# Optimization experiments

Hardware: AMD Instinct MI355X
Metric: run time of the kernel (lower is better)

## Reference

```python
import jax, jax.numpy as jnp
from jax import lax
import numpy as np

N, T, V, C, K, NIN, TSTEPS = 4096, 1, 26, 256, 3, 9, 25


def setup_inputs() -> dict:
    key = jax.random.key(0)
    ks = jax.random.split(key, 28)
    s = 0.02
    inp = {
        "inputs": jax.random.normal(ks[0], (N, T, V * 3), jnp.float32),
        "inputs_previous": jax.random.normal(ks[1], (N, T, V * 3), jnp.float32),
        "inputs_previous2": jax.random.normal(ks[2], (N, T, V * 3), jnp.float32),
        "hidden": jax.random.normal(ks[3], (N, C, V), jnp.float32),
        # graph adjacency buffer [k_num, V, V] (non-trainable) + edge weights
        "A": jax.random.uniform(ks[4], (K, V, V), jnp.float32),
        "emul": jnp.ones((K, V, V), jnp.float32),
        "eadd": jnp.ones((K, V, V), jnp.float32),
        # DecodeGcn conv1d kernel_size=1 -> stored as [C*K, C] matrix
        "conv_w": jax.random.normal(ks[5], (C * K, C), jnp.float32) * s,
        "conv_b": jnp.zeros((C * K,), jnp.float32),
        # GRU input projections (bias=True), Linear(n_in_dec=9 -> C)
        "Wir": jax.random.normal(ks[6], (C, NIN), jnp.float32) * s,
        "bir": jnp.zeros((C,), jnp.float32),
        "Wii": jax.random.normal(ks[7], (C, NIN), jnp.float32) * s,
        "bii": jnp.zeros((C,), jnp.float32),
        "Win": jax.random.normal(ks[8], (C, NIN), jnp.float32) * s,
        "b_in": jnp.zeros((C,), jnp.float32),
        # GRU hidden projections (bias=False)
        "Whr": jax.random.normal(ks[9], (C, C), jnp.float32) * s,
        "Whi": jax.random.normal(ks[10], (C, C), jnp.float32) * s,
        "Whh": jax.random.normal(ks[11], (C, C), jnp.float32) * s,
        # output MLP head
        "W1": jax.random.normal(ks[12], (C, C), jnp.float32) * s,
        "b1": jnp.zeros((C,), jnp.float32),
        "W2": jax.random.normal(ks[13], (C, C), jnp.float32) * s,
        "b2": jnp.zeros((C,), jnp.float32),
        "W3": jax.random.normal(ks[14], (3, C), jnp.float32) * s,
        "b3": jnp.zeros((3,), jnp.float32),
        "t": TSTEPS,
    }
    return inp


def reference(inputs, inputs_previous, inputs_previous2, hidden, A, emul, eadd,
              conv_w, conv_b, Wir, bir, Wii, bii, Win, b_in, Whr, Whi, Whh,
              W1, b1, W2, b2, W3, b3, t):
    n_batch, n_t, d = inputs.shape
    v = A.shape[1]
    k_num = A.shape[0]
    c = hidden.shape[1]

    x0 = inputs.reshape(n_batch, n_t, v, -1)[:, 0]            # [N,V,3]
    xp = inputs_previous.reshape(n_batch, n_t, v, -1)[:, 0]   # [N,V,3]
    xp2 = inputs_previous2.reshape(n_batch, n_t, v, -1)[:, 0]  # [N,V,3]

    A_adj = A * emul + eadd  # [k,V,V]
    # noise injected on position channels each step (torch.randn * 0.0005)
    noise = jax.random.normal(jax.random.key(1), (t, n_batch, v, 3), jnp.float32) * 5e-4

    def gcn(h):  # h: [N,C,V] -> [N,C,V]   (kernel-size-1 conv + graph einsum)
        y = jnp.einsum('ncv,oc->nov', h, conv_w) + conv_b[None, :, None]  # [N,C*k,V]
        y = y.reshape(n_batch, k_num, c, v)
        return jnp.einsum('nkcv,kvw->ncw', y, A_adj)

    def step(carry, inp):
        hid, h1, h2, h3 = carry  # hid: [N,C,V]; h1/h2/h3: last three predictions [N,V,3]
        s, nz = inp
        msg = lax.cond(s < 10, gcn, lambda h: h, hid)  # [N,C,V]
        # unified history recurrence (covers step 0/1/2/>=3 branches):
        ins_p = h1
        ins_v = h2 - h3
        ins_a = ins_p - h2 - ins_v
        x = jnp.concatenate([ins_p + nz, ins_v, ins_a], axis=-1)  # [N,V,9]
        m = msg.transpose(0, 2, 1)       # [N,V,C]
        hprev = hid.transpose(0, 2, 1)   # [N,V,C]
        r = jax.nn.sigmoid(x @ Wir.T + bir + m @ Whr.T)
        z = jax.nn.sigmoid(x @ Wii.T + bii + m @ Whi.T)
        nn_ = jnp.tanh(x @ Win.T + b_in + r * (m @ Whh.T))
        hnew = (1.0 - z) * nn_ + z * hprev  # [N,V,C]
        # output MLP (dropout in eval mode = identity), leaky_relu slope 0.1
        hd = jax.nn.leaky_relu(hnew @ W1.T + b1, 0.1)
        hd = jax.nn.leaky_relu(hd @ W2.T + b2, 0.1)
        res = hd @ W3.T + b3                 # [N,V,3]
        pred = x[:, :, :3] + res             # pred_ = (ins_p + noise) + residual
        return (hnew.transpose(0, 2, 1), pred, h1, h2), pred

    init = (hidden, x0, xp, xp2)
    _, preds = lax.scan(step, init, (jnp.arange(t), noise))  # preds: [t,N,V,3]
    return preds.transpose(1, 2, 0, 3)  # [N,V,t,3] == preds.transpose(1,2) in torch
```

## Files before the change

kernel.cpp:

```cpp
#include <hip/hip_runtime.h>

#define M_ROWS 106496
#define NBATCH 4096
#define VN 26
#define KNUM 3
#define TS 25

typedef unsigned short u16;
typedef __attribute__((ext_vector_type(8))) short v8s;
typedef __attribute__((ext_vector_type(4))) float v4f;

__device__ __forceinline__ u16 f2bf(float f) {
    unsigned u = __float_as_uint(f);
    u += 0x7FFF + ((u >> 16) & 1);
    return (u16)(u >> 16);
}
__device__ __forceinline__ float bf2f(u16 h) {
    return __uint_as_float(((unsigned)h) << 16);
}
__device__ __forceinline__ float sigm(float x) {
    return 1.f / (1.f + __expf(-x));
}
__device__ __forceinline__ float tanh_fast(float x) {
    return 2.f / (1.f + __expf(-2.f * x)) - 1.f;
}

typedef const __attribute__((address_space(1))) unsigned int* gas_t;
typedef __attribute__((address_space(3))) unsigned int* las_t;
__device__ __forceinline__ void gl16(const void* g, void* l) {
    __builtin_amdgcn_global_load_lds((gas_t)g, (las_t)l, 16, 0, 0);
}

template <int ACT>
__global__ __launch_bounds__(256) void gemm_nt(
    const u16* __restrict__ A, const u16* __restrict__ Bt,
    const float* __restrict__ bias, u16* __restrict__ C, int nc)
{
    __shared__ u16 Al[2][128 * 32];
    __shared__ u16 Bl[2][128 * 32];
    const int m0 = blockIdx.x * 128;
    const int n0 = blockIdx.y * 128;
    const int tid = threadIdx.x;
    const int wid = tid >> 6, lane = tid & 63;
    const int ln = lane & 15, q = lane >> 4;
    const int qs8 = (q ^ ((ln >> 1) & 3)) * 8;
    const int wm = (wid >> 1) * 64, wn = (wid & 1) * 64;
    const int srow = tid >> 2;
    const int spart = (tid & 3) ^ ((srow >> 1) & 3);

    const u16* gA0 = &A[(size_t)(m0 + srow) * 256 + spart * 8];
    const u16* gB0 = &Bt[(size_t)(n0 + srow) * 256 + spart * 8];

#define STG(b, kk) do {                                                     \
        gl16(gA0 + (kk) * 32,            &Al[b][wid * 512]);                \
        gl16(gA0 + 64 * 256 + (kk) * 32, &Al[b][2048 + wid * 512]);         \
        gl16(gB0 + (kk) * 32,            &Bl[b][wid * 512]);                \
        gl16(gB0 + 64 * 256 + (kk) * 32, &Bl[b][2048 + wid * 512]);         \
    } while (0)

    v4f acc[4][4] = {};
    STG(0, 0);
    __syncthreads();
#pragma unroll
    for (int kt = 0; kt < 8; ++kt) {
        const int cb = kt & 1, nb = cb ^ 1;
        if (kt < 7) STG(nb, kt + 1);
        v8s af[4], bfv[4];
#pragma unroll
        for (int i = 0; i < 4; ++i)
            af[i] = *(const v8s*)&Al[cb][(wm + i * 16 + ln) * 32 + qs8];
#pragma unroll
        for (int j = 0; j < 4; ++j)
            bfv[j] = *(const v8s*)&Bl[cb][(wn + j * 16 + ln) * 32 + qs8];
#pragma unroll
        for (int i = 0; i < 4; ++i)
#pragma unroll
            for (int j = 0; j < 4; ++j)
                acc[i][j] = __builtin_amdgcn_mfma_f32_16x16x32_bf16(
                    af[i], bfv[j], acc[i][j], 0, 0, 0);
        __syncthreads();
    }
#undef STG
#pragma unroll
    for (int i = 0; i < 4; ++i)
#pragma unroll
        for (int j = 0; j < 4; ++j) {
            int gc = n0 + wn + j * 16 + ln;
            float b = bias[gc];
#pragma unroll
            for (int r = 0; r < 4; ++r) {
                int gr = m0 + wm + i * 16 + q * 4 + r;
                float v = acc[i][j][r] + b;
                if (ACT) v = v > 0.f ? v : 0.1f * v;
                C[(size_t)gr * nc + gc] = f2bf(v);
            }
        }
}

__global__ __launch_bounds__(256) void gemm_head(
    const u16* __restrict__ A, const u16* __restrict__ Bt,
    const float* __restrict__ bias, const float* __restrict__ w3,
    float* __restrict__ resp0, float* __restrict__ resp1)
{
    __shared__ u16 Al[2][128 * 32];
    __shared__ u16 Bl[2][128 * 32];
    __shared__ float w3l[3 * 128];
    __shared__ float resl[2][128][3];
    const int m0 = blockIdx.x * 128;
    const int by = blockIdx.y;
    const int n0 = by * 128;
    const int tid = threadIdx.x;
    const int wid = tid >> 6, lane = tid & 63;
    const int ln = lane & 15, q = lane >> 4;
    const int qs8 = (q ^ ((ln >> 1) & 3)) * 8;
    const int wm = (wid >> 1) * 64, wn = (wid & 1) * 64;
    const int wnh = wid & 1;
    const int srow = tid >> 2;
    const int spart = (tid & 3) ^ ((srow >> 1) & 3);

    for (int idx = tid; idx < 384; idx += 256)
        w3l[idx] = w3[(idx >> 7) * 256 + n0 + (idx & 127)];

    const u16* gA0 = &A[(size_t)(m0 + srow) * 256 + spart * 8];
    const u16* gB0 = &Bt[(size_t)(n0 + srow) * 256 + spart * 8];

#define STG(b, kk) do {                                                     \
        gl16(gA0 + (kk) * 32,            &Al[b][wid * 512]);                \
        gl16(gA0 + 64 * 256 + (kk) * 32, &Al[b][2048 + wid * 512]);         \
        gl16(gB0 + (kk) * 32,            &Bl[b][wid * 512]);                \
        gl16(gB0 + 64 * 256 + (kk) * 32, &Bl[b][2048 + wid * 512]);         \
    } while (0)

    v4f acc[4][4] = {};
    STG(0, 0);
    __syncthreads();
#pragma unroll
    for (int kt = 0; kt < 8; ++kt) {
        const int cb = kt & 1, nb = cb ^ 1;
        if (kt < 7) STG(nb, kt + 1);
        v8s af[4], bfv[4];
#pragma unroll
        for (int i = 0; i < 4; ++i)
            af[i] = *(const v8s*)&Al[cb][(wm + i * 16 + ln) * 32 + qs8];
#pragma unroll
        for (int j = 0; j < 4; ++j)
            bfv[j] = *(const v8s*)&Bl[cb][(wn + j * 16 + ln) * 32 + qs8];
#pragma unroll
        for (int i = 0; i < 4; ++i)
#pragma unroll
            for (int j = 0; j < 4; ++j)
                acc[i][j] = __builtin_amdgcn_mfma_f32_16x16x32_bf16(
                    af[i], bfv[j], acc[i][j], 0, 0, 0);
        __syncthreads();
    }
#undef STG

    float bj[4], wv[3][4];
#pragma unroll
    for (int j = 0; j < 4; ++j) {
        bj[j] = bias[n0 + wn + j * 16 + ln];
#pragma unroll
        for (int t = 0; t < 3; ++t)
            wv[t][j] = w3l[t * 128 + wn + j * 16 + ln];
    }
#pragma unroll
    for (int i = 0; i < 4; ++i) {
        float part[3][4] = {};
#pragma unroll
        for (int j = 0; j < 4; ++j)
#pragma unroll
            for (int r = 0; r < 4; ++r) {
                float v = acc[i][j][r] + bj[j];
                v = v > 0.f ? v : 0.1f * v;
                part[0][r] += v * wv[0][j];
                part[1][r] += v * wv[1][j];
                part[2][r] += v * wv[2][j];
            }
#pragma unroll
        for (int off = 1; off < 16; off <<= 1)
#pragma unroll
            for (int t = 0; t < 3; ++t)
#pragma unroll
                for (int r = 0; r < 4; ++r)
                    part[t][r] += __shfl_xor(part[t][r], off, 16);
        if (ln == 0) {
            int row = wm + i * 16 + q * 4;
#pragma unroll
            for (int r = 0; r < 4; ++r)
#pragma unroll
                for (int t = 0; t < 3; ++t)
                    resl[wnh][row + r][t] = part[t][r];
        }
    }
    __syncthreads();
    float* rp = by ? resp1 : resp0;
    for (int idx = tid; idx < 384; idx += 256) {
        int t = idx >> 7, row = idx & 127;
        rp[(size_t)(m0 + row) * 3 + t] = resl[0][row][t] + resl[1][row][t];
    }
}

__global__ __launch_bounds__(256) void head_fin(
    const float* __restrict__ resp0, const float* __restrict__ resp1,
    const float* __restrict__ b3, const float* __restrict__ p1,
    const float* __restrict__ p2, float* __restrict__ pnew,
    u16* __restrict__ xpad, float* __restrict__ out, int s)
{
    int m = blockIdx.x * 256 + threadIdx.x;
    float s0 = resp0[m * 3 + 0] + resp1[m * 3 + 0];
    float s1 = resp0[m * 3 + 1] + resp1[m * 3 + 1];
    float s2 = resp0[m * 3 + 2] + resp1[m * 3 + 2];
    float a0 = p1[m * 3 + 0], a1 = p1[m * 3 + 1], a2 = p1[m * 3 + 2];
    float c0 = p2[m * 3 + 0], c1 = p2[m * 3 + 1], c2 = p2[m * 3 + 2];
    float o0 = a0 + s0 + b3[0];
    float o1 = a1 + s1 + b3[1];
    float o2 = a2 + s2 + b3[2];
    size_t ob = ((size_t)m * TS + s) * 3;
    out[ob + 0] = o0; out[ob + 1] = o1; out[ob + 2] = o2;
    pnew[m * 3 + 0] = o0; pnew[m * 3 + 1] = o1; pnew[m * 3 + 2] = o2;
    unsigned t[32];
#pragma unroll
    for (int i = 0; i < 32; ++i) t[i] = 0;
    t[0] = f2bf(o0); t[1] = f2bf(o1); t[2] = f2bf(o2);
    t[3] = f2bf(a0 - c0); t[4] = f2bf(a1 - c1); t[5] = f2bf(a2 - c2);
    t[6] = f2bf(o0 - 2.f * a0 + c0);
    t[7] = f2bf(o1 - 2.f * a1 + c1);
    t[8] = f2bf(o2 - 2.f * a2 + c2);
    t[9] = f2bf(1.f);
    uint4* dst = (uint4*)&xpad[(size_t)m * 32];
#pragma unroll
    for (int wq = 0; wq < 4; ++wq) {
        uint4 u;
        u.x = t[wq * 8 + 0] | (t[wq * 8 + 1] << 16);
        u.y = t[wq * 8 + 2] | (t[wq * 8 + 3] << 16);
        u.z = t[wq * 8 + 4] | (t[wq * 8 + 5] << 16);
        u.w = t[wq * 8 + 6] | (t[wq * 8 + 7] << 16);
        dst[wq] = u;
    }
}

__global__ __launch_bounds__(256) void graph_mix(
    const u16* __restrict__ y, const float* __restrict__ aadj,
    u16* __restrict__ msg)
{
    __shared__ u16 yl[VN * 768];
    const int n = blockIdx.x, tid = threadIdx.x;
    const uint4* src = (const uint4*)(y + (size_t)n * VN * 768);
    for (int idx = tid; idx < VN * 768 / 8; idx += 256)
        ((uint4*)yl)[idx] = src[idx];
    __syncthreads();
    const int c = tid;
    float acc[VN] = {};
    for (int k = 0; k < KNUM; ++k)
        for (int v = 0; v < VN; ++v) {
            float yv = bf2f(yl[v * 768 + k * 256 + c]);
            const float* ap = &aadj[(k * VN + v) * VN];
#pragma unroll
            for (int w = 0; w < VN; ++w) acc[w] += yv * ap[w];
        }
    size_t base = (size_t)n * VN * 256;
    for (int w = 0; w < VN; ++w) msg[base + w * 256 + c] = f2bf(acc[w]);
}

__global__ __launch_bounds__(256) void gru_fused(
    const u16* __restrict__ Am, const u16* __restrict__ xpad,
    const u16* __restrict__ hprev, u16* __restrict__ hout,
    const u16* __restrict__ wfull, const u16* __restrict__ wxn)
{
    __shared__ u16 Al[128 * 32];
    __shared__ u16 Bl[192 * 32];
    __shared__ u16 Xl[64 * 32];
    const int m0 = blockIdx.x * 128;
    const int n0 = blockIdx.y * 64;
    const int tid = threadIdx.x;
    const int wid = tid >> 6, lane = tid & 63;
    const int ln = lane & 15, q = lane >> 4;
    const int qs8 = (q ^ ((ln >> 1) & 3)) * 8;
    const int wm = (wid >> 1) * 64, wn = (wid & 1) * 32;
    const int srow = tid >> 2;
    const int spart = (tid & 3) ^ ((srow >> 1) & 3);

    gl16(&wxn[(size_t)(n0 + srow) * 32 + spart * 8], &Xl[(wid * 64) * 8]);

    v4f accr[4][2] = {}, accz[4][2] = {}, acch[4][2] = {}, accn[4][2] = {};

    for (int kt = 0; kt < 9; ++kt) {
#pragma unroll
        for (int p = 0; p < 2; ++p) {
            const u16* ga = (kt < 8)
                ? &Am[(size_t)(m0 + p * 64 + srow) * 256 + kt * 32 + spart * 8]
                : &xpad[(size_t)(m0 + p * 64 + srow) * 32 + spart * 8];
            gl16(ga, &Al[(p * 256 + wid * 64) * 8]);
        }
#pragma unroll
        for (int p = 0; p < 3; ++p)
            gl16(&wfull[(size_t)(p * 256 + n0 + srow) * 288 + kt * 32 + spart * 8],
                 &Bl[(p * 256 + wid * 64) * 8]);
        __syncthreads();

        v8s af[4];
#pragma unroll
        for (int i = 0; i < 4; ++i)
            af[i] = *(const v8s*)&Al[(wm + i * 16 + ln) * 32 + qs8];
        v8s bfr[3][2];
#pragma unroll
        for (int g = 0; g < 3; ++g)
#pragma unroll
            for (int j = 0; j < 2; ++j)
                bfr[g][j] = *(const v8s*)&Bl[(g * 64 + wn + j * 16 + ln) * 32 + qs8];
#pragma unroll
        for (int i = 0; i < 4; ++i)
#pragma unroll
            for (int j = 0; j < 2; ++j) {
                accr[i][j] = __builtin_amdgcn_mfma_f32_16x16x32_bf16(af[i], bfr[0][j], accr[i][j], 0, 0, 0);
                accz[i][j] = __builtin_amdgcn_mfma_f32_16x16x32_bf16(af[i], bfr[1][j], accz[i][j], 0, 0, 0);
                acch[i][j] = __builtin_amdgcn_mfma_f32_16x16x32_bf16(af[i], bfr[2][j], acch[i][j], 0, 0, 0);
            }
        if (kt == 8) {
            v8s bfn[2];
#pragma unroll
            for (int j = 0; j < 2; ++j)
                bfn[j] = *(const v8s*)&Xl[(wn + j * 16 + ln) * 32 + qs8];
#pragma unroll
            for (int i = 0; i < 4; ++i)
#pragma unroll
                for (int j = 0; j < 2; ++j)
                    accn[i][j] = __builtin_amdgcn_mfma_f32_16x16x32_bf16(af[i], bfn[j], accn[i][j], 0, 0, 0);
        }
        __syncthreads();
    }

#pragma unroll
    for (int i = 0; i < 4; ++i)
#pragma unroll
        for (int j = 0; j < 2; ++j) {
            int gc = n0 + wn + j * 16 + ln;
#pragma unroll
            for (int r = 0; r < 4; ++r) {
                int gr = m0 + wm + i * 16 + q * 4 + r;
                float rg = sigm(accr[i][j][r]);
                float zg = sigm(accz[i][j][r]);
                float nn = tanh_fast(accn[i][j][r] + rg * acch[i][j][r]);
                float hp = bf2f(hprev[(size_t)gr * 256 + gc]);
                hout[(size_t)gr * 256 + gc] = f2bf((1.f - zg) * nn + zg * hp);
            }
        }
}

__global__ __launch_bounds__(256) void init_xpad(
    const float* __restrict__ x0, const float* __restrict__ xp,
    const float* __restrict__ xp2, u16* __restrict__ xpad)
{
    int m = blockIdx.x * 256 + threadIdx.x;
    float a0 = x0[m * 3 + 0], a1 = x0[m * 3 + 1], a2 = x0[m * 3 + 2];
    float b0 = xp[m * 3 + 0], b1 = xp[m * 3 + 1], b2 = xp[m * 3 + 2];
    float c0 = xp2[m * 3 + 0], c1 = xp2[m * 3 + 1], c2 = xp2[m * 3 + 2];
    unsigned t[32];
#pragma unroll
    for (int i = 0; i < 32; ++i) t[i] = 0;
    t[0] = f2bf(a0); t[1] = f2bf(a1); t[2] = f2bf(a2);
    t[3] = f2bf(b0 - c0); t[4] = f2bf(b1 - c1); t[5] = f2bf(b2 - c2);
    t[6] = f2bf(a0 - 2.f * b0 + c0);
    t[7] = f2bf(a1 - 2.f * b1 + c1);
    t[8] = f2bf(a2 - 2.f * b2 + c2);
    t[9] = f2bf(1.f);
    uint4* dst = (uint4*)&xpad[(size_t)m * 32];
#pragma unroll
    for (int wq = 0; wq < 4; ++wq) {
        uint4 u;
        u.x = t[wq * 8 + 0] | (t[wq * 8 + 1] << 16);
        u.y = t[wq * 8 + 2] | (t[wq * 8 + 3] << 16);
        u.z = t[wq * 8 + 4] | (t[wq * 8 + 5] << 16);
        u.w = t[wq * 8 + 6] | (t[wq * 8 + 7] << 16);
        dst[wq] = u;
    }
}

__global__ __launch_bounds__(256) void transpose_h(
    const float* __restrict__ hidden, u16* __restrict__ hA)
{
    __shared__ float hl[256 * VN];
    const int n = blockIdx.x, tid = threadIdx.x;
    const uint4* src = (const uint4*)(hidden + (size_t)n * 256 * VN);
    for (int idx = tid; idx < 256 * VN / 4; idx += 256)
        ((uint4*)hl)[idx] = src[idx];
    __syncthreads();
    size_t base = (size_t)n * VN * 256;
    for (int idx = tid; idx < VN * 256; idx += 256) {
        int v = idx >> 8, c = idx & 255;
        hA[base + idx] = f2bf(hl[c * VN + v]);
    }
}

__global__ __launch_bounds__(256) void pack_weights(
    const float* __restrict__ Whr, const float* __restrict__ Whi,
    const float* __restrict__ Whh, const float* __restrict__ convw_f,
    const float* __restrict__ W1f, const float* __restrict__ W2f,
    const float* __restrict__ Af, const float* __restrict__ emul,
    const float* __restrict__ eadd, const float* __restrict__ Wir,
    const float* __restrict__ Wii, const float* __restrict__ Win,
    const float* __restrict__ bir, const float* __restrict__ bii,
    const float* __restrict__ b_in, const float* __restrict__ convb_f,
    const float* __restrict__ b1f, const float* __restrict__ b2f,
    const float* __restrict__ W3f, const float* __restrict__ b3f,
    u16* __restrict__ wfull, u16* __restrict__ wxn, u16* __restrict__ convw,
    u16* __restrict__ w1, u16* __restrict__ w2, float* __restrict__ aadj,
    float* __restrict__ convb, float* __restrict__ b1, float* __restrict__ b2,
    float* __restrict__ w3, float* __restrict__ b3)
{
    int gid = blockIdx.x * 256 + threadIdx.x;
    int stride = gridDim.x * 256;
    for (int i = gid; i < 768 * 288; i += stride) {
        int row = i / 288, col = i - row * 288;
        int g = row >> 8, c = row & 255;
        float v = 0.f;
        if (col < 256)
            v = (g == 0 ? Whr : (g == 1 ? Whi : Whh))[c * 256 + col];
        else if (col < 265) {
            int tcol = col - 256;
            v = (g == 0 ? Wir[c * 9 + tcol] : (g == 1 ? Wii[c * 9 + tcol] : 0.f));
        } else if (col == 265)
            v = (g == 0 ? bir[c] : (g == 1 ? bii[c] : 0.f));
        wfull[i] = f2bf(v);
    }
    for (int i = gid; i < 256 * 32; i += stride) {
        int c = i >> 5, col = i & 31;
        float v = 0.f;
        if (col < 9) v = Win[c * 9 + col];
        else if (col == 9) v = b_in[c];
        wxn[i] = f2bf(v);
    }
    for (int i = gid; i < 65536; i += stride) {
        w1[i] = f2bf(W1f[i]);
        w2[i] = f2bf(W2f[i]);
    }
    for (int i = gid; i < 196608; i += stride) convw[i] = f2bf(convw_f[i]);
    for (int i = gid; i < KNUM * VN * VN; i += stride)
        aadj[i] = Af[i] * emul[i] + eadd[i];
    for (int i = gid; i < 256; i += stride) { b1[i] = b1f[i]; b2[i] = b2f[i]; }
    for (int i = gid; i < 768; i += stride) { convb[i] = convb_f[i]; w3[i] = W3f[i]; }
    if (gid < 3) b3[gid] = b3f[gid];
}

extern "C" void kernel_launch(void* const* d_in, const int* in_sizes, int n_in,
                              void* d_out, int out_size, void* d_ws, size_t ws_size,
                              hipStream_t stream)
{
    const float* inputs   = (const float*)d_in[0];
    const float* inputs_p = (const float*)d_in[1];
    const float* inputs_p2= (const float*)d_in[2];
    const float* hidden   = (const float*)d_in[3];
    const float* Af       = (const float*)d_in[4];
    const float* emul     = (const float*)d_in[5];
    const float* eadd     = (const float*)d_in[6];
    const float* conv_w   = (const float*)d_in[7];
    const float* conv_b   = (const float*)d_in[8];
    const float* Wir      = (const float*)d_in[9];
    const float* bir      = (const float*)d_in[10];
    const float* Wii      = (const float*)d_in[11];
    const float* bii      = (const float*)d_in[12];
    const float* Win      = (const float*)d_in[13];
    const float* b_in     = (const float*)d_in[14];
    const float* Whr      = (const float*)d_in[15];
    const float* Whi      = (const float*)d_in[16];
    const float* Whh      = (const float*)d_in[17];
    const float* W1f      = (const float*)d_in[18];
    const float* b1f      = (const float*)d_in[19];
    const float* W2f      = (const float*)d_in[20];
    const float* b2f      = (const float*)d_in[21];
    const float* W3f      = (const float*)d_in[22];
    const float* b3f      = (const float*)d_in[23];
    float* out = (float*)d_out;

    const size_t M = M_ROWS;
    char* ws = (char*)d_ws;
    size_t off = 0;
    auto alloc = [&](size_t bytes) -> void* {
        void* p = ws + off;
        off = (off + bytes + 255) & ~(size_t)255;
        return p;
    };
    u16* hA    = (u16*)alloc(M * 256 * 2);
    u16* hB    = (u16*)alloc(M * 256 * 2);
    u16* msg   = (u16*)alloc(M * 256 * 2);
    u16* ybuf  = (u16*)alloc(M * 768 * 2);
    u16* xpad  = (u16*)alloc(M * 32 * 2);
    float* pa  = (float*)alloc(M * 3 * 4);
    float* pb  = (float*)alloc(M * 3 * 4);
    float* pc  = (float*)alloc(M * 3 * 4);
    float* rs0 = (float*)alloc(M * 3 * 4);
    float* rs1 = (float*)alloc(M * 3 * 4);
    u16* wfull = (u16*)alloc(768 * 288 * 2);
    u16* wxn   = (u16*)alloc(256 * 32 * 2);
    u16* convw = (u16*)alloc(196608 * 2);
    u16* w1    = (u16*)alloc(65536 * 2);
    u16* w2    = (u16*)alloc(65536 * 2);
    float* aadj  = (float*)alloc(KNUM * VN * VN * 4);
    float* convb = (float*)alloc(768 * 4);
    float* b1    = (float*)alloc(256 * 4);
    float* b2    = (float*)alloc(256 * 4);
    float* w3    = (float*)alloc(768 * 4);
    float* b3    = (float*)alloc(16);
    if (off > ws_size) return;

    pack_weights<<<512, 256, 0, stream>>>(
        Whr, Whi, Whh, conv_w, W1f, W2f, Af, emul, eadd, Wir, Wii, Win,
        bir, bii, b_in, conv_b, b1f, b2f, W3f, b3f,
        wfull, wxn, convw, w1, w2, aadj, convb, b1, b2, w3, b3);
    transpose_h<<<NBATCH, 256, 0, stream>>>(hidden, hA);
    init_xpad<<<M_ROWS / 256, 256, 0, stream>>>(inputs, inputs_p, inputs_p2, xpad);
    hipMemcpyAsync(pa, inputs,    M * 3 * 4, hipMemcpyDeviceToDevice, stream);
    hipMemcpyAsync(pb, inputs_p,  M * 3 * 4, hipMemcpyDeviceToDevice, stream);
    hipMemcpyAsync(pc, inputs_p2, M * 3 * 4, hipMemcpyDeviceToDevice, stream);

    u16* hcur = hA;  u16* hnext = hB;
    float* P1 = pa;  float* P2 = pb;  float* P3 = pc;
    u16* hd  = ybuf;
    const int MB = M_ROWS / 128;

    for (int s = 0; s < TS; ++s) {
        const u16* m_ptr;
        if (s < 10) {
            gemm_nt<0><<<dim3(MB, 6), 256, 0, stream>>>(hcur, convw, convb, ybuf, 768);
            graph_mix<<<NBATCH, 256, 0, stream>>>(ybuf, aadj, msg);
            m_ptr = msg;
        } else {
            m_ptr = hcur;
        }
        gru_fused<<<dim3(MB, 4), 256, 0, stream>>>(m_ptr, xpad, hcur, hnext,
                                                   wfull, wxn);
        gemm_nt<1><<<dim3(MB, 2), 256, 0, stream>>>(hnext, w1, b1, hd, 256);
        gemm_head<<<dim3(MB, 2), 256, 0, stream>>>(hd, w2, b2, w3, rs0, rs1);
        head_fin<<<M_ROWS / 256, 256, 0, stream>>>(rs0, rs1, b3, P1, P2, P3,
                                                   xpad, out, s);
        float* t = P3; P3 = P2; P2 = P1; P1 = t;
        u16* ht = hcur; hcur = hnext; hnext = ht;
    }
}
```

Before: 6.412 ms.

## Fuse W1 GEMM, W2 GEMM, W3 head and finalization into one MLP kernel

Replaces the three per-step kernels (W1 GEMM writing hd to global, W2 GEMM with W3 reduction writing partial sums, and head_fin) with a single mlp_head kernel. Each block handles 64 rows across the full 256 columns. The first-layer activations stay in a swizzled LDS buffer and feed the second GEMM directly. This removes the global round trip of the 106496x256 hidden activation, the partial-sum buffers, and two launches per step. In exchange, every block re-streams both full weight matrices, uses more LDS (about 56KB), which may limit occupancy, and only 64 threads do the final epilogue.

```diff
diff --git a/kernel.cpp b/kernel.cpp
--- a/kernel.cpp
+++ b/kernel.cpp
@@ -97,145 +97,177 @@
         }
 }
 
-__global__ __launch_bounds__(256) void gemm_head(
-    const u16* __restrict__ A, const u16* __restrict__ Bt,
-    const float* __restrict__ bias, const float* __restrict__ w3,
-    float* __restrict__ resp0, float* __restrict__ resp1)
-{
-    __shared__ u16 Al[2][128 * 32];
-    __shared__ u16 Bl[2][128 * 32];
-    __shared__ float w3l[3 * 128];
-    __shared__ float resl[2][128][3];
-    const int m0 = blockIdx.x * 128;
-    const int by = blockIdx.y;
-    const int n0 = by * 128;
+__global__ __launch_bounds__(256) void mlp_head(
+    const u16* __restrict__ A, const u16* __restrict__ w1,
+    const float* __restrict__ b1, const u16* __restrict__ w2,
+    const float* __restrict__ b2, const float* __restrict__ w3,
+    const float* __restrict__ b3, const float* __restrict__ p1,
+    const float* __restrict__ p2, float* __restrict__ pnew,
+    u16* __restrict__ xpad, float* __restrict__ out, int s)
+{
+    __shared__ u16 Ast[2][64 * 32];
+    __shared__ u16 Bst[2][256 * 32];
+    __shared__ u16 hdl[64 * 256];
+    __shared__ float resl[2][64][3];
+    const int m0 = blockIdx.x * 64;
     const int tid = threadIdx.x;
     const int wid = tid >> 6, lane = tid & 63;
     const int ln = lane & 15, q = lane >> 4;
     const int qs8 = (q ^ ((ln >> 1) & 3)) * 8;
-    const int wm = (wid >> 1) * 64, wn = (wid & 1) * 64;
+    const int wm = (wid >> 1) * 32;
+    const int wn = (wid & 1) * 128;
     const int wnh = wid & 1;
     const int srow = tid >> 2;
     const int spart = (tid & 3) ^ ((srow >> 1) & 3);
 
-    for (int idx = tid; idx < 384; idx += 256)
-        w3l[idx] = w3[(idx >> 7) * 256 + n0 + (idx & 127)];
-
     const u16* gA0 = &A[(size_t)(m0 + srow) * 256 + spart * 8];
-    const u16* gB0 = &Bt[(size_t)(n0 + srow) * 256 + spart * 8];
-
-#define STG(b, kk) do {                                                     \
-        gl16(gA0 + (kk) * 32,            &Al[b][wid * 512]);                \
-        gl16(gA0 + 64 * 256 + (kk) * 32, &Al[b][2048 + wid * 512]);         \
-        gl16(gB0 + (kk) * 32,            &Bl[b][wid * 512]);                \
-        gl16(gB0 + 64 * 256 + (kk) * 32, &Bl[b][2048 + wid * 512]);         \
+    const u16* gW1 = &w1[(size_t)srow * 256 + spart * 8];
+    const u16* gW2 = &w2[(size_t)srow * 256 + spart * 8];
+
+#define STGA(b, kk) gl16(gA0 + (kk) * 32, &Ast[b][wid * 512])
+#define STGB(b, kk, W) do {                                                 \
+        gl16(W + (kk) * 32,             &Bst[b][wid * 512]);                \
+        gl16(W + 64 * 256 + (kk) * 32,  &Bst[b][2048 + wid * 512]);         \
+        gl16(W + 128 * 256 + (kk) * 32, &Bst[b][4096 + wid * 512]);         \
+        gl16(W + 192 * 256 + (kk) * 32, &Bst[b][6144 + wid * 512]);         \
     } while (0)
 
-    v4f acc[4][4] = {};
-    STG(0, 0);
+    v4f acc[2][8] = {};
+    STGA(0, 0); STGB(0, 0, gW1);
     __syncthreads();
-#pragma unroll
     for (int kt = 0; kt < 8; ++kt) {
         const int cb = kt & 1, nb = cb ^ 1;
-        if (kt < 7) STG(nb, kt + 1);
-        v8s af[4], bfv[4];
-#pragma unroll
-        for (int i = 0; i < 4; ++i)
-            af[i] = *(const v8s*)&Al[cb][(wm + i * 16 + ln) * 32 + qs8];
-#pragma unroll
-        for (int j = 0; j < 4; ++j)
-            bfv[j] = *(const v8s*)&Bl[cb][(wn + j * 16 + ln) * 32 + qs8];
-#pragma unroll
-        for (int i = 0; i < 4; ++i)
-#pragma unroll
-            for (int j = 0; j < 4; ++j)
+        if (kt < 7) { STGA(nb, kt + 1); STGB(nb, kt + 1, gW1); }
+        else        { STGB(nb, 0, gW2); }
+        v8s af[2], bf[8];
+#pragma unroll
+        for (int i = 0; i < 2; ++i)
+            af[i] = *(const v8s*)&Ast[cb][(wm + i * 16 + ln) * 32 + qs8];
+#pragma unroll
+        for (int j = 0; j < 8; ++j)
+            bf[j] = *(const v8s*)&Bst[cb][(wn + j * 16 + ln) * 32 + qs8];
+#pragma unroll
+        for (int i = 0; i < 2; ++i)
+#pragma unroll
+            for (int j = 0; j < 8; ++j)
                 acc[i][j] = __builtin_amdgcn_mfma_f32_16x16x32_bf16(
-                    af[i], bfv[j], acc[i][j], 0, 0, 0);
+                    af[i], bf[j], acc[i][j], 0, 0, 0);
         __syncthreads();
     }
-#undef STG
-
-    float bj[4], wv[3][4];
-#pragma unroll
-    for (int j = 0; j < 4; ++j) {
-        bj[j] = bias[n0 + wn + j * 16 + ln];
+
+#pragma unroll
+    for (int i = 0; i < 2; ++i)
+#pragma unroll
+        for (int j = 0; j < 8; ++j) {
+            int col = wn + j * 16 + ln;
+            float bb = b1[col];
+#pragma unroll
+            for (int r = 0; r < 4; ++r) {
+                int row = wm + i * 16 + q * 4 + r;
+                float v = acc[i][j][r] + bb;
+                v = v > 0.f ? v : 0.1f * v;
+                int ch = (col >> 3) ^ (row & 15);
+                hdl[row * 256 + ch * 8 + (col & 7)] = f2bf(v);
+            }
+        }
+    __syncthreads();
+
+    v4f acc2[2][8] = {};
+    for (int kt = 0; kt < 8; ++kt) {
+        const int cb = kt & 1, nb = cb ^ 1;
+        if (kt < 7) STGB(nb, kt + 1, gW2);
+        v8s af[2], bf[8];
+#pragma unroll
+        for (int i = 0; i < 2; ++i) {
+            int row = wm + i * 16 + ln;
+            int ch = (kt * 4 + q) ^ (row & 15);
+            af[i] = *(const v8s*)&hdl[row * 256 + ch * 8];
+        }
+#pragma unroll
+        for (int j = 0; j < 8; ++j)
+            bf[j] = *(const v8s*)&Bst[cb][(wn + j * 16 + ln) * 32 + qs8];
+#pragma unroll
+        for (int i = 0; i < 2; ++i)
+#pragma unroll
+            for (int j = 0; j < 8; ++j)
+                acc2[i][j] = __builtin_amdgcn_mfma_f32_16x16x32_bf16(
+                    af[i], bf[j], acc2[i][j], 0, 0, 0);
+        __syncthreads();
+    }
+#undef STGA
+#undef STGB
+
+    float part[3][2][4] = {};
+#pragma unroll
+    for (int j = 0; j < 8; ++j) {
+        int col = wn + j * 16 + ln;
+        float bb = b2[col];
+        float w30 = w3[col], w31 = w3[256 + col], w32 = w3[512 + col];
+#pragma unroll
+        for (int i = 0; i < 2; ++i)
+#pragma unroll
+            for (int r = 0; r < 4; ++r) {
+                float v = acc2[i][j][r] + bb;
+                v = v > 0.f ? v : 0.1f * v;
+                part[0][i][r] += v * w30;
+                part[1][i][r] += v * w31;
+                part[2][i][r] += v * w32;
+            }
+    }
+#pragma unroll
+    for (int off = 1; off < 16; off <<= 1)
 #pragma unroll
         for (int t = 0; t < 3; ++t)
-            wv[t][j] = w3l[t * 128 + wn + j * 16 + ln];
-    }
-#pragma unroll
-    for (int i = 0; i < 4; ++i) {
-        float part[3][4] = {};
-#pragma unroll
-        for (int j = 0; j < 4; ++j)
+#pragma unroll
+            for (int i = 0; i < 2; ++i)
+#pragma unroll
+                for (int r = 0; r < 4; ++r)
+                    part[t][i][r] += __shfl_xor(part[t][i][r], off, 16);
+    if (ln == 0) {
+#pragma unroll
+        for (int i = 0; i < 2; ++i)
 #pragma unroll
             for (int r = 0; r < 4; ++r) {
-                float v = acc[i][j][r] + bj[j];
-                v = v > 0.f ? v : 0.1f * v;
-                part[0][r] += v * wv[0][j];
-                part[1][r] += v * wv[1][j];
-                part[2][r] += v * wv[2][j];
+                int row = wm + i * 16 + q * 4 + r;
+#pragma unroll
+                for (int t = 0; t < 3; ++t)
+                    resl[wnh][row][t] = part[t][i][r];
             }
-#pragma unroll
-        for (int off = 1; off < 16; off <<= 1)
-#pragma unroll
-            for (int t = 0; t < 3; ++t)
-#pragma unroll
-                for (int r = 0; r < 4; ++r)
-                    part[t][r] += __shfl_xor(part[t][r], off, 16);
-        if (ln == 0) {
-            int row = wm + i * 16 + q * 4;
-#pragma unroll
-            for (int r = 0; r < 4; ++r)
-#pragma unroll
-                for (int t = 0; t < 3; ++t)
-                    resl[wnh][row + r][t] = part[t][r];
-        }
     }
     __syncthreads();
-    float* rp = by ? resp1 : resp0;
-    for (int idx = tid; idx < 384; idx += 256) {
-        int t = idx >> 7, row = idx & 127;
-        rp[(size_t)(m0 + row) * 3 + t] = resl[0][row][t] + resl[1][row][t];
-    }
-}
-
-__global__ __launch_bounds__(256) void head_fin(
-    const float* __restrict__ resp0, const float* __restrict__ resp1,
-    const float* __restrict__ b3, const float* __restrict__ p1,
-    const float* __restrict__ p2, float* __restrict__ pnew,
-    u16* __restrict__ xpad, float* __restrict__ out, int s)
-{
-    int m = blockIdx.x * 256 + threadIdx.x;
-    float s0 = resp0[m * 3 + 0] + resp1[m * 3 + 0];
-    float s1 = resp0[m * 3 + 1] + resp1[m * 3 + 1];
-    float s2 = resp0[m * 3 + 2] + resp1[m * 3 + 2];
-    float a0 = p1[m * 3 + 0], a1 = p1[m * 3 + 1], a2 = p1[m * 3 + 2];
-    float c0 = p2[m * 3 + 0], c1 = p2[m * 3 + 1], c2 = p2[m * 3 + 2];
-    float o0 = a0 + s0 + b3[0];
-    float o1 = a1 + s1 + b3[1];
-    float o2 = a2 + s2 + b3[2];
-    size_t ob = ((size_t)m * TS + s) * 3;
-    out[ob + 0] = o0; out[ob + 1] = o1; out[ob + 2] = o2;
-    pnew[m * 3 + 0] = o0; pnew[m * 3 + 1] = o1; pnew[m * 3 + 2] = o2;
-    unsigned t[32];
-#pragma unroll
-    for (int i = 0; i < 32; ++i) t[i] = 0;
-    t[0] = f2bf(o0); t[1] = f2bf(o1); t[2] = f2bf(o2);
-    t[3] = f2bf(a0 - c0); t[4] = f2bf(a1 - c1); t[5] = f2bf(a2 - c2);
-    t[6] = f2bf(o0 - 2.f * a0 + c0);
-    t[7] = f2bf(o1 - 2.f * a1 + c1);
-    t[8] = f2bf(o2 - 2.f * a2 + c2);
-    t[9] = f2bf(1.f);
-    uint4* dst = (uint4*)&xpad[(size_t)m * 32];
-#pragma unroll
-    for (int wq = 0; wq < 4; ++wq) {
-        uint4 u;
-        u.x = t[wq * 8 + 0] | (t[wq * 8 + 1] << 16);
-        u.y = t[wq * 8 + 2] | (t[wq * 8 + 3] << 16);
-        u.z = t[wq * 8 + 4] | (t[wq * 8 + 5] << 16);
-        u.w = t[wq * 8 + 6] | (t[wq * 8 + 7] << 16);
-        dst[wq] = u;
+
+    if (tid < 64) {
+        int m = m0 + tid;
+        float s0 = resl[0][tid][0] + resl[1][tid][0];
+        float s1 = resl[0][tid][1] + resl[1][tid][1];
+        float s2 = resl[0][tid][2] + resl[1][tid][2];
+        float a0 = p1[m * 3 + 0], a1 = p1[m * 3 + 1], a2 = p1[m * 3 + 2];
+        float c0 = p2[m * 3 + 0], c1 = p2[m * 3 + 1], c2 = p2[m * 3 + 2];
+        float o0 = a0 + s0 + b3[0];
+        float o1 = a1 + s1 + b3[1];
+        float o2 = a2 + s2 + b3[2];
+        size_t ob = ((size_t)m * TS + s) * 3;
+        out[ob + 0] = o0; out[ob + 1] = o1; out[ob + 2] = o2;
+        pnew[m * 3 + 0] = o0; pnew[m * 3 + 1] = o1; pnew[m * 3 + 2] = o2;
+        unsigned t[32];
+#pragma unroll
+        for (int i = 0; i < 32; ++i) t[i] = 0;
+        t[0] = f2bf(o0); t[1] = f2bf(o1); t[2] = f2bf(o2);
+        t[3] = f2bf(a0 - c0); t[4] = f2bf(a1 - c1); t[5] = f2bf(a2 - c2);
+        t[6] = f2bf(o0 - 2.f * a0 + c0);
+        t[7] = f2bf(o1 - 2.f * a1 + c1);
+        t[8] = f2bf(o2 - 2.f * a2 + c2);
+        t[9] = f2bf(1.f);
+        uint4* dst = (uint4*)&xpad[(size_t)m * 32];
+#pragma unroll
+        for (int wq = 0; wq < 4; ++wq) {
+            uint4 u;
+            u.x = t[wq * 8 + 0] | (t[wq * 8 + 1] << 16);
+            u.y = t[wq * 8 + 2] | (t[wq * 8 + 3] << 16);
+            u.z = t[wq * 8 + 4] | (t[wq * 8 + 5] << 16);
+            u.w = t[wq * 8 + 6] | (t[wq * 8 + 7] << 16);
+            dst[wq] = u;
+        }
     }
 }
 
@@ -488,8 +520,6 @@
     float* pa  = (float*)alloc(M * 3 * 4);
     float* pb  = (float*)alloc(M * 3 * 4);
     float* pc  = (float*)alloc(M * 3 * 4);
-    float* rs0 = (float*)alloc(M * 3 * 4);
-    float* rs1 = (float*)alloc(M * 3 * 4);
     u16* wfull = (u16*)alloc(768 * 288 * 2);
     u16* wxn   = (u16*)alloc(256 * 32 * 2);
     u16* convw = (u16*)alloc(196608 * 2);
@@ -515,7 +545,6 @@
 
     u16* hcur = hA;  u16* hnext = hB;
     float* P1 = pa;  float* P2 = pb;  float* P3 = pc;
-    u16* hd  = ybuf;
     const int MB = M_ROWS / 128;
 
     for (int s = 0; s < TS; ++s) {
@@ -529,10 +558,8 @@
         }
         gru_fused<<<dim3(MB, 4), 256, 0, stream>>>(m_ptr, xpad, hcur, hnext,
                                                    wfull, wxn);
-        gemm_nt<1><<<dim3(MB, 2), 256, 0, stream>>>(hnext, w1, b1, hd, 256);
-        gemm_head<<<dim3(MB, 2), 256, 0, stream>>>(hd, w2, b2, w3, rs0, rs1);
-        head_fin<<<M_ROWS / 256, 256, 0, stream>>>(rs0, rs1, b3, P1, P2, P3,
-                                                   xpad, out, s);
+        mlp_head<<<M_ROWS / 64, 256, 0, stream>>>(hnext, w1, b1, w2, b2, w3, b3,
+                                                  P1, P2, P3, xpad, out, s);
         float* t = P3; P3 = P2; P2 = P1; P1 = t;
         u16* ht = hcur; hcur = hnext; hnext = ht;
     }
```

Measured after the change: 6.020 ms. 1.07x faster.
